# Kernel optimization log

Measured on AMD Instinct MI355X. Metric: run time of the kernel, lower is better.

Reference implementation:

```python
import jax, jax.numpy as jnp
import numpy as np

N = 8192
F_IN = 512
F_OUT = 64
ALPHA = 0.2  # LeakyReLU negative slope
MASK_VAL = -9e15


def setup_inputs() -> dict:
    key = jax.random.key(0)
    k1, k2, k3, k4, k5 = jax.random.split(key, 5)
    x = jax.random.normal(k1, (N, F_IN), dtype=jnp.float32)
    adj = jax.random.randint(k2, (N, N), 0, 2, dtype=jnp.int32)
    # params: W uniform(-stdv, stdv) per reset_parameters, A xavier-ish
    stdv = 1.0 / np.sqrt(F_OUT)
    W = jax.random.uniform(k3, (F_IN, F_OUT), dtype=jnp.float32, minval=-stdv, maxval=stdv)
    bias = jax.random.uniform(k4, (F_OUT,), dtype=jnp.float32, minval=-stdv, maxval=stdv)
    A = jax.random.normal(k5, (2 * F_OUT, 1), dtype=jnp.float32) * 0.1
    return {"x": x, "adj": adj, "W": W, "bias": bias, "A": A}


def reference(x, adj, W, bias, A):
    # Wh: [N, F_OUT]
    Wh = x @ W
    # e_ij = leakyrelu([Wh_i || Wh_j] @ A) == leakyrelu(Wh_i @ a1 + Wh_j @ a2)
    # (mathematically identical to the N x N x 2F concat, without materializing it)
    a1 = A[:F_OUT, 0]  # [F_OUT]
    a2 = A[F_OUT:, 0]  # [F_OUT]
    s1 = Wh @ a1  # [N]
    s2 = Wh @ a2  # [N]
    e = jax.nn.leaky_relu(s1[:, None] + s2[None, :], negative_slope=ALPHA)  # [N, N]
    masked = jnp.where(adj > 0, e, MASK_VAL)
    attention = jax.nn.softmax(masked, axis=1)  # [N, N]
    # dropout p=0.0 -> identity
    out = attention @ Wh + bias  # [N, F_OUT]
    return out
```

## Files before the change

### kernel.cpp

```cpp
#include <hip/hip_runtime.h>

#define NN 8192
#define FIN 512
#define FOUT 64
#define LRELU_ALPHA 0.2f
#define MASK_VALF -9000000000000000.0f

typedef __attribute__((ext_vector_type(4))) float f32x4;
typedef __attribute__((ext_vector_type(4))) int i32x4;
typedef __attribute__((ext_vector_type(8))) __bf16 bf16x8;

__global__ __launch_bounds__(256) void gat_wh(
    const float* __restrict__ x, const float* __restrict__ W,
    const float* __restrict__ A,
    __bf16* __restrict__ WhbT, float* __restrict__ s1, float* __restrict__ s2)
{
    const int gid = blockIdx.x * 256 + threadIdx.x;
    const int row = gid >> 4;
    const int cg  = gid & 15;

    f32x4 acc = {0.f, 0.f, 0.f, 0.f};
    const float* xrow = x + (size_t)row * FIN;
    const float* wcol = W + cg * 4;

    #pragma unroll 2
    for (int k = 0; k < FIN; k += 4) {
        f32x4 xv = *reinterpret_cast<const f32x4*>(xrow + k);
        #pragma unroll
        for (int u = 0; u < 4; ++u) {
            f32x4 wv = *reinterpret_cast<const f32x4*>(wcol + (size_t)(k + u) * FOUT);
            acc += xv[u] * wv;
        }
    }

    f32x4 a1v = *reinterpret_cast<const f32x4*>(A + cg * 4);
    f32x4 a2v = *reinterpret_cast<const f32x4*>(A + FOUT + cg * 4);
    float s1p = acc[0]*a1v[0] + acc[1]*a1v[1] + acc[2]*a1v[2] + acc[3]*a1v[3];
    float s2p = acc[0]*a2v[0] + acc[1]*a2v[1] + acc[2]*a2v[2] + acc[3]*a2v[3];
    #pragma unroll
    for (int off = 1; off < 16; off <<= 1) {
        s1p += __shfl_xor(s1p, off);
        s2p += __shfl_xor(s2p, off);
    }
    if (cg == 0) { s1[row] = s1p; s2[row] = s2p; }

    #pragma unroll
    for (int u = 0; u < 4; ++u)
        WhbT[(size_t)(cg * 4 + u) * NN + row] = (__bf16)acc[u];
}

__global__ __launch_bounds__(256) void gat_attn(
    const int* __restrict__ adj, const __bf16* __restrict__ WhbT,
    const float* __restrict__ s1g, const float* __restrict__ s2g,
    const float* __restrict__ bias, float* __restrict__ out)
{
    __shared__ float s2_lds[NN];
    __shared__ float om[4][16];
    __shared__ float ol[4][16];
    __shared__ float oacc[4][16][FOUT];

    const int tid  = threadIdx.x;
    const int w    = tid >> 6;
    const int lane = tid & 63;
    const int r    = lane & 15;
    const int q    = lane >> 4;
    const int row0 = blockIdx.x * 16;

    for (int i = tid; i < NN / 4; i += 256)
        reinterpret_cast<f32x4*>(s2_lds)[i] = reinterpret_cast<const f32x4*>(s2g)[i];
    __syncthreads();

    const float s1r = s1g[row0 + r];

    float m = -INFINITY;
    float l = 0.0f;
    f32x4 acc0 = {0,0,0,0}, acc1 = {0,0,0,0}, acc2 = {0,0,0,0}, acc3 = {0,0,0,0};

    const int*    adjp = adj + (size_t)(row0 + r) * NN + q * 8;
    const __bf16* wp   = WhbT + q * 8;

    for (int it = 0; it < 64; ++it) {
        const int j0 = (w << 11) + (it << 5);

        i32x4 av0 = *reinterpret_cast<const i32x4*>(adjp + j0);
        i32x4 av1 = *reinterpret_cast<const i32x4*>(adjp + j0 + 4);
        bf16x8 b0 = *reinterpret_cast<const bf16x8*>(wp + (size_t)(0 * 16 + r) * NN + j0);
        bf16x8 b1 = *reinterpret_cast<const bf16x8*>(wp + (size_t)(1 * 16 + r) * NN + j0);
        bf16x8 b2 = *reinterpret_cast<const bf16x8*>(wp + (size_t)(2 * 16 + r) * NN + j0);
        bf16x8 b3 = *reinterpret_cast<const bf16x8*>(wp + (size_t)(3 * 16 + r) * NN + j0);
        f32x4 s2a = *reinterpret_cast<const f32x4*>(s2_lds + j0 + q * 8);
        f32x4 s2b = *reinterpret_cast<const f32x4*>(s2_lds + j0 + q * 8 + 4);

        float ev[8];
        #pragma unroll
        for (int i = 0; i < 4; ++i) {
            float t0 = s1r + s2a[i];
            float e0 = fmaxf(t0, LRELU_ALPHA * t0);
            ev[i] = (av0[i] > 0) ? e0 : MASK_VALF;
            float t1 = s1r + s2b[i];
            float e1 = fmaxf(t1, LRELU_ALPHA * t1);
            ev[i + 4] = (av1[i] > 0) ? e1 : MASK_VALF;
        }

        float tmax = ev[0];
        #pragma unroll
        for (int i = 1; i < 8; ++i) tmax = fmaxf(tmax, ev[i]);
        tmax = fmaxf(tmax, __shfl_xor(tmax, 16));
        tmax = fmaxf(tmax, __shfl_xor(tmax, 32));

        const float mnew  = fmaxf(m, tmax);
        const float alpha = __expf(m - mnew);
        m = mnew;

        float psum = 0.f;
        bf16x8 af;
        #pragma unroll
        for (int i = 0; i < 8; ++i) {
            float p = __expf(ev[i] - mnew);
            psum += p;
            af[i] = (__bf16)p;
        }
        psum += __shfl_xor(psum, 16);
        psum += __shfl_xor(psum, 32);
        l = l * alpha + psum;

        const float ar0 = __shfl(alpha, q * 4 + 0);
        const float ar1 = __shfl(alpha, q * 4 + 1);
        const float ar2 = __shfl(alpha, q * 4 + 2);
        const float ar3 = __shfl(alpha, q * 4 + 3);
        f32x4 av = {ar0, ar1, ar2, ar3};
        acc0 *= av; acc1 *= av; acc2 *= av; acc3 *= av;

        acc0 = __builtin_amdgcn_mfma_f32_16x16x32_bf16(af, b0, acc0, 0, 0, 0);
        acc1 = __builtin_amdgcn_mfma_f32_16x16x32_bf16(af, b1, acc1, 0, 0, 0);
        acc2 = __builtin_amdgcn_mfma_f32_16x16x32_bf16(af, b2, acc2, 0, 0, 0);
        acc3 = __builtin_amdgcn_mfma_f32_16x16x32_bf16(af, b3, acc3, 0, 0, 0);
    }

    if (lane < 16) { om[w][lane] = m; ol[w][lane] = l; }
    #pragma unroll
    for (int reg = 0; reg < 4; ++reg) {
        oacc[w][q * 4 + reg][0 * 16 + r] = acc0[reg];
        oacc[w][q * 4 + reg][1 * 16 + r] = acc1[reg];
        oacc[w][q * 4 + reg][2 * 16 + r] = acc2[reg];
        oacc[w][q * 4 + reg][3 * 16 + r] = acc3[reg];
    }
    __syncthreads();

    for (int o = tid; o < 16 * FOUT; o += 256) {
        const int rr = o >> 6;
        const int f  = o & 63;
        const float M = fmaxf(fmaxf(om[0][rr], om[1][rr]), fmaxf(om[2][rr], om[3][rr]));
        float L = 0.f, O = 0.f;
        #pragma unroll
        for (int w2 = 0; w2 < 4; ++w2) {
            const float sc = __expf(om[w2][rr] - M);
            L += sc * ol[w2][rr];
            O += sc * oacc[w2][rr][f];
        }
        out[(size_t)(row0 + rr) * FOUT + f] = O / L + bias[f];
    }
}

extern "C" void kernel_launch(void* const* d_in, const int* in_sizes, int n_in,
                              void* d_out, int out_size, void* d_ws, size_t ws_size,
                              hipStream_t stream)
{
    const float* x    = (const float*)d_in[0];
    const int*   adj  = (const int*)d_in[1];
    const float* W    = (const float*)d_in[2];
    const float* bias = (const float*)d_in[3];
    const float* A    = (const float*)d_in[4];
    float* out = (float*)d_out;

    char* ws = (char*)d_ws;
    __bf16* WhbT = (__bf16*)ws;
    float*  s1   = (float*)(ws + (size_t)FOUT * NN * sizeof(__bf16));
    float*  s2   = s1 + NN;

    gat_wh<<<dim3(NN * 16 / 256), dim3(256), 0, stream>>>(x, W, A, WhbT, s1, s2);
    gat_attn<<<dim3(NN / 16), dim3(256), 0, stream>>>(adj, WhbT, s1, s2, bias, out);
}
```

Baseline: 456.2 us.

## Replace online softmax with a precomputed per-row max bound and widen to 8 waves

Computes the global max of s2 once per block and uses leakyrelu(s1_i + max s2) as a fixed upper bound on each row's logit. Because of that bound, the running-max rescaling, per-iteration cross-lane max and sum shuffles, and accumulator multiplies can all be dropped. Masked entries now become zero probabilities directly. The block grows to 512 threads, with 8 waves each covering 1024 columns, and s2 is read from global memory instead of being staged in LDS. In exchange, exponentials can underflow when a row's real max sits far below the bound, and a fully masked row now outputs only the bias instead of a uniform average.

```diff
diff --git a/kernel.cpp b/kernel.cpp
--- a/kernel.cpp
+++ b/kernel.cpp
@@ -4,7 +4,6 @@
 #define FIN 512
 #define FOUT 64
 #define LRELU_ALPHA 0.2f
-#define MASK_VALF -9000000000000000.0f
 
 typedef __attribute__((ext_vector_type(4))) float f32x4;
 typedef __attribute__((ext_vector_type(4))) int i32x4;
@@ -49,15 +48,14 @@
         WhbT[(size_t)(cg * 4 + u) * NN + row] = (__bf16)acc[u];
 }
 
-__global__ __launch_bounds__(256) void gat_attn(
+__global__ __launch_bounds__(512) void gat_attn(
     const int* __restrict__ adj, const __bf16* __restrict__ WhbT,
     const float* __restrict__ s1g, const float* __restrict__ s2g,
     const float* __restrict__ bias, float* __restrict__ out)
 {
-    __shared__ float s2_lds[NN];
-    __shared__ float om[4][16];
-    __shared__ float ol[4][16];
-    __shared__ float oacc[4][16][FOUT];
+    __shared__ float red[8];
+    __shared__ float ol[8][16];
+    __shared__ float oacc[8][16][FOUT];
 
     const int tid  = threadIdx.x;
     const int w    = tid >> 6;
@@ -66,21 +64,31 @@
     const int q    = lane >> 4;
     const int row0 = blockIdx.x * 16;
 
-    for (int i = tid; i < NN / 4; i += 256)
-        reinterpret_cast<f32x4*>(s2_lds)[i] = reinterpret_cast<const f32x4*>(s2g)[i];
+    float mloc = -INFINITY;
+    for (int i = tid; i < NN; i += 512) mloc = fmaxf(mloc, s2g[i]);
+    #pragma unroll
+    for (int off = 32; off >= 1; off >>= 1) mloc = fmaxf(mloc, __shfl_xor(mloc, off));
+    if (lane == 0) red[w] = mloc;
     __syncthreads();
+    float s2max = red[0];
+    #pragma unroll
+    for (int i = 1; i < 8; ++i) s2max = fmaxf(s2max, red[i]);
 
-    const float s1r = s1g[row0 + r];
+    const float s1r  = s1g[row0 + r];
+    const float th   = s1r + s2max;
+    const float mhat = fmaxf(th, LRELU_ALPHA * th);
 
-    float m = -INFINITY;
-    float l = 0.0f;
+    float lsum = 0.0f;
     f32x4 acc0 = {0,0,0,0}, acc1 = {0,0,0,0}, acc2 = {0,0,0,0}, acc3 = {0,0,0,0};
 
-    const int*    adjp = adj + (size_t)(row0 + r) * NN + q * 8;
-    const __bf16* wp   = WhbT + q * 8;
+    const int     cbase = (w << 10) + (q << 3);
+    const int*    adjp  = adj + (size_t)(row0 + r) * NN + cbase;
+    const __bf16* wp    = WhbT + cbase;
+    const float*  s2p   = s2g + cbase;
 
-    for (int it = 0; it < 64; ++it) {
-        const int j0 = (w << 11) + (it << 5);
+    #pragma unroll 2
+    for (int it = 0; it < 32; ++it) {
+        const int j0 = it << 5;
 
         i32x4 av0 = *reinterpret_cast<const i32x4*>(adjp + j0);
         i32x4 av1 = *reinterpret_cast<const i32x4*>(adjp + j0 + 4);
@@ -88,48 +96,28 @@
         bf16x8 b1 = *reinterpret_cast<const bf16x8*>(wp + (size_t)(1 * 16 + r) * NN + j0);
         bf16x8 b2 = *reinterpret_cast<const bf16x8*>(wp + (size_t)(2 * 16 + r) * NN + j0);
         bf16x8 b3 = *reinterpret_cast<const bf16x8*>(wp + (size_t)(3 * 16 + r) * NN + j0);
-        f32x4 s2a = *reinterpret_cast<const f32x4*>(s2_lds + j0 + q * 8);
-        f32x4 s2b = *reinterpret_cast<const f32x4*>(s2_lds + j0 + q * 8 + 4);
+        f32x4 s2a = *reinterpret_cast<const f32x4*>(s2p + j0);
+        f32x4 s2b = *reinterpret_cast<const f32x4*>(s2p + j0 + 4);
 
-        float ev[8];
+        bf16x8 af;
+        float ps = 0.0f;
         #pragma unroll
         for (int i = 0; i < 4; ++i) {
             float t0 = s1r + s2a[i];
             float e0 = fmaxf(t0, LRELU_ALPHA * t0);
-            ev[i] = (av0[i] > 0) ? e0 : MASK_VALF;
+            float p0 = __expf(e0 - mhat);
+            p0 = (av0[i] > 0) ? p0 : 0.0f;
+            ps += p0;
+            af[i] = (__bf16)p0;
+
             float t1 = s1r + s2b[i];
             float e1 = fmaxf(t1, LRELU_ALPHA * t1);
-            ev[i + 4] = (av1[i] > 0) ? e1 : MASK_VALF;
+            float p1 = __expf(e1 - mhat);
+            p1 = (av1[i] > 0) ? p1 : 0.0f;
+            ps += p1;
+            af[i + 4] = (__bf16)p1;
         }
-
-        float tmax = ev[0];
-        #pragma unroll
-        for (int i = 1; i < 8; ++i) tmax = fmaxf(tmax, ev[i]);
-        tmax = fmaxf(tmax, __shfl_xor(tmax, 16));
-        tmax = fmaxf(tmax, __shfl_xor(tmax, 32));
-
-        const float mnew  = fmaxf(m, tmax);
-        const float alpha = __expf(m - mnew);
-        m = mnew;
-
-        float psum = 0.f;
-        bf16x8 af;
-        #pragma unroll
-        for (int i = 0; i < 8; ++i) {
-            float p = __expf(ev[i] - mnew);
-            psum += p;
-            af[i] = (__bf16)p;
-        }
-        psum += __shfl_xor(psum, 16);
-        psum += __shfl_xor(psum, 32);
-        l = l * alpha + psum;
-
-        const float ar0 = __shfl(alpha, q * 4 + 0);
-        const float ar1 = __shfl(alpha, q * 4 + 1);
-        const float ar2 = __shfl(alpha, q * 4 + 2);
-        const float ar3 = __shfl(alpha, q * 4 + 3);
-        f32x4 av = {ar0, ar1, ar2, ar3};
-        acc0 *= av; acc1 *= av; acc2 *= av; acc3 *= av;
+        lsum += ps;
 
         acc0 = __builtin_amdgcn_mfma_f32_16x16x32_bf16(af, b0, acc0, 0, 0, 0);
         acc1 = __builtin_amdgcn_mfma_f32_16x16x32_bf16(af, b1, acc1, 0, 0, 0);
@@ -137,7 +125,10 @@
         acc3 = __builtin_amdgcn_mfma_f32_16x16x32_bf16(af, b3, acc3, 0, 0, 0);
     }
 
-    if (lane < 16) { om[w][lane] = m; ol[w][lane] = l; }
+    lsum += __shfl_xor(lsum, 16);
+    lsum += __shfl_xor(lsum, 32);
+    if (lane < 16) ol[w][r] = lsum;
+
     #pragma unroll
     for (int reg = 0; reg < 4; ++reg) {
         oacc[w][q * 4 + reg][0 * 16 + r] = acc0[reg];
@@ -147,17 +138,16 @@
     }
     __syncthreads();
 
-    for (int o = tid; o < 16 * FOUT; o += 256) {
+    for (int o = tid; o < 16 * FOUT; o += 512) {
         const int rr = o >> 6;
         const int f  = o & 63;
-        const float M = fmaxf(fmaxf(om[0][rr], om[1][rr]), fmaxf(om[2][rr], om[3][rr]));
-        float L = 0.f, O = 0.f;
+        float L = 0.0f, O = 0.0f;
         #pragma unroll
-        for (int w2 = 0; w2 < 4; ++w2) {
-            const float sc = __expf(om[w2][rr] - M);
-            L += sc * ol[w2][rr];
-            O += sc * oacc[w2][rr][f];
+        for (int w2 = 0; w2 < 8; ++w2) {
+            L += ol[w2][rr];
+            O += oacc[w2][rr][f];
         }
+        L = (L > 0.0f) ? L : 1.0f;
         out[(size_t)(row0 + rr) * FOUT + f] = O / L + bias[f];
     }
 }
@@ -179,5 +169,5 @@
     float*  s2   = s1 + NN;
 
     gat_wh<<<dim3(NN * 16 / 256), dim3(256), 0, stream>>>(x, W, A, WhbT, s1, s2);
-    gat_attn<<<dim3(NN / 16), dim3(256), 0, stream>>>(adj, WhbT, s1, s2, bias, out);
+    gat_attn<<<dim3(NN / 16), dim3(512), 0, stream>>>(adj, WhbT, s1, s2, bias, out);
 }
```

New measurement: 461.0 us. Within noise of the previous version (+1.1%).
